# Performance work log

Hardware: AMD Instinct MI355X
Metric: run time of the kernel (lower is better)

## Reference

```python
import jax, jax.numpy as jnp
import numpy as np

N_QUBITS = 12
N_LAYERS = 6
BATCH = 512
DIM = 2 ** N_QUBITS


def _apply_1q(psi, G, wire):
    """Apply a single-qubit gate on `wire` (wire 0 = most significant).
    psi: [B, 2^n] complex. G: [2,2] (shared) or [B,2,2] (batched)."""
    B = psi.shape[0]
    left = 2 ** wire
    psi = psi.reshape(B, left, 2, -1)
    if G.ndim == 2:
        psi = jnp.einsum('ij,bxjy->bxiy', G, psi)
    else:
        psi = jnp.einsum('bij,bxjy->bxiy', G, psi)
    return psi.reshape(B, -1)


def _apply_cnot(psi, c, t):
    """CNOT with control c, target t on [B, 2^n] state."""
    B = psi.shape[0]
    ps = psi.reshape((B,) + (2,) * N_QUBITS)
    ca, ta = c + 1, t + 1
    c0 = jnp.take(ps, 0, axis=ca)
    c1 = jnp.take(ps, 1, axis=ca)
    flip_ax = ta if ta < ca else ta - 1
    c1 = jnp.flip(c1, axis=flip_ax)  # X on target within control=1 block
    ps = jnp.stack([c0, c1], axis=ca)
    return ps.reshape(B, -1)


def _circuit(x, weights):
    B = x.shape[0]
    psi = jnp.zeros((B, DIM), jnp.complex64).at[:, 0].set(1.0)

    # AngleEmbedding: RY(x_w) on each wire (batched gate matrices)
    h = 0.5 * x
    c, s = jnp.cos(h).astype(jnp.complex64), jnp.sin(h).astype(jnp.complex64)
    for w in range(N_QUBITS):
        G = jnp.stack([jnp.stack([c[:, w], -s[:, w]], -1),
                       jnp.stack([s[:, w], c[:, w]], -1)], -2)  # [B,2,2]
        psi = _apply_1q(psi, G, w)

    # StronglyEntanglingLayers: Rot(phi,theta,omega) per wire, then ring of CNOTs
    for l in range(N_LAYERS):
        phi, theta, omega = weights[l, :, 0], weights[l, :, 1], weights[l, :, 2]
        ct = jnp.cos(0.5 * theta).astype(jnp.complex64)
        st = jnp.sin(0.5 * theta).astype(jnp.complex64)
        ep = jnp.exp(-0.5j * (phi + omega).astype(jnp.complex64))
        em = jnp.exp(0.5j * (phi - omega).astype(jnp.complex64))
        # Rot = RZ(omega) RY(theta) RZ(phi)
        m00 = ep * ct
        m01 = -em * st
        m10 = jnp.conj(em) * st
        m11 = jnp.conj(ep) * ct
        for w in range(N_QUBITS):
            G = jnp.array([[m00[w], m01[w]], [m10[w], m11[w]]], jnp.complex64)
            psi = _apply_1q(psi, G, w)
        r = l % (N_QUBITS - 1) + 1
        for w in range(N_QUBITS):
            psi = _apply_cnot(psi, w, (w + r) % N_QUBITS)

    # <Z_w> for every wire
    probs = psi.real ** 2 + psi.imag ** 2  # [B, 2^n]
    exps = []
    for w in range(N_QUBITS):
        p = probs.reshape(B, 2 ** w, 2, -1)
        exps.append(p[:, :, 0, :].sum((1, 2)) - p[:, :, 1, :].sum((1, 2)))
    return jnp.stack(exps, -1)  # [B, n_qubits]


def setup_inputs() -> dict:
    key = jax.random.key(0)
    k1, k2, k3, k4 = jax.random.split(key, 4)
    x = jax.random.uniform(k1, (BATCH, N_QUBITS), jnp.float32, -np.pi, np.pi)
    weights = jax.random.uniform(k2, (N_LAYERS, N_QUBITS, 3), jnp.float32, 0.0, 2.0 * np.pi)
    W = jax.random.normal(k3, (1, N_QUBITS), jnp.float32) * 0.3
    b = jax.random.normal(k4, (1,), jnp.float32) * 0.01
    return {"x": x, "weights": weights, "W": W, "b": b}


def reference(x, weights, W, b):
    z = _circuit(x, weights)              # [B, n_qubits]
    y = z @ W.T + b                       # [B, 1]
    return y.squeeze(-1)                  # [B]
```

## Files before the change

kernel.cpp:

```cpp
#include <hip/hip_runtime.h>
#include <stdint.h>

#define NQ 12
#define DIM 4096
#define NLAYERS 6
#define TPB 512

typedef float v2f __attribute__((ext_vector_type(2)));

struct Pass_t {
    uint32_t WT[9];
    uint32_t WL[4];
    uint32_t RT[9];
    uint32_t RL[8];
};
struct Pass9_t {
    uint32_t WT[6];
    uint32_t WL[4];
    uint32_t RT[6];
    uint32_t RL[8];
};
struct CK_t {
    Pass9_t PA1;
    Pass9_t PA2;
    Pass_t PB;
    Pass_t P1[NLAYERS];
    uint32_t frow[NQ];
};

constexpr uint32_t S1f(uint32_t k){ return (k & 0xFC0u) | ((k & 7u) << 3) | ((k >> 3) & 7u); }
constexpr uint32_t S2f(uint32_t k){ return (k & 0xE38u) | ((k & 7u) << 6) | ((k >> 6) & 7u); }
constexpr uint32_t S3f(uint32_t k){ return (k & 0x1F8u) | ((k & 7u) << 9) | ((k >> 9) & 7u); }

constexpr uint32_t ech_reduce(const uint32_t* v, int n, uint32_t x){
    bool ch = true;
    while (ch) {
        ch = false;
        for (int i = 0; i < n; i++)
            if (v[i] && (x ^ v[i]) < x) { x ^= v[i]; ch = true; }
    }
    return x;
}

constexpr Pass_t build_pass(const uint32_t* Mc) {
    Pass_t P{};
    uint32_t rows[12]{};
    rows[0] = 4u;
    int nr = 1;
    uint32_t full[12]{}; int nf = 0; full[nf++] = 4u;
    uint32_t We[4]{};  int nw = 0;
    uint32_t Re[5]{};  int nre = 0;
    {
        uint32_t p0 = 0;
        for (int j = 0; j < 5; j++)
            p0 |= (uint32_t)(__builtin_popcount(4u & Mc[3 + j]) & 1) << j;
        uint32_t r = ech_reduce(Re, nre, p0);
        if (r) Re[nre++] = r;
    }
    for (int slot = 0; slot < 4; slot++) {
        uint32_t chosen = 0;
        for (int relax = 0; relax < 3 && !chosen; relax++) {
            for (uint32_t m = 1; m < 4096u && !chosen; m++) {
                if (m & 4u) continue;
                uint32_t wp = (m >> 3) & 15u;
                uint32_t wr = ech_reduce(We, nw, wp);
                if (relax < 2 && !wr) continue;
                uint32_t rp = 0;
                for (int j = 0; j < 5; j++)
                    rp |= (uint32_t)(__builtin_popcount(m & Mc[3 + j]) & 1) << j;
                uint32_t rr = ech_reduce(Re, nre, rp);
                if (relax < 1 && !rr) continue;
                uint32_t fr = ech_reduce(full, nf, m);
                if (!fr) continue;
                chosen = m; full[nf++] = fr;
                if (wr && nw < 4) We[nw++] = wr;
                if (rr && nre < 5) Re[nre++] = rr;
            }
        }
        rows[nr++] = chosen;
    }
    for (int slot = nr; slot < 12; slot++) {
        for (uint32_t m = 1; m < 4096u; m++) {
            if (m & 4u) continue;
            uint32_t fr = ech_reduce(full, nf, m);
            if (fr) { rows[slot] = m; full[nf++] = fr; break; }
        }
    }
    uint32_t col[12]{}, lmc[12]{};
    for (int j = 0; j < 12; j++) {
        uint32_t c = 0;
        for (int i = 0; i < 12; i++) c |= (uint32_t)((rows[i] >> j) & 1u) << i;
        col[j] = c;
    }
    for (int j = 0; j < 12; j++) {
        uint32_t a = 0, mc = Mc[j];
        for (int q = 0; q < 12; q++) if ((mc >> q) & 1u) a ^= col[q];
        lmc[j] = a;
    }
    for (int j = 0; j < 9; j++) { P.WT[j] = col[3 + j]; P.RT[j] = lmc[3 + j]; }
    for (int j = 0; j < 4; j++) {
        uint32_t a = 0;
        for (int q = 0; q < 2; q++) if ((j >> q) & 1) a ^= col[q];
        P.WL[j] = a;
    }
    for (int l = 0; l < 8; l++) {
        uint32_t a = 0;
        for (int q = 0; q < 3; q++) if ((l >> q) & 1) a ^= lmc[q];
        P.RL[l] = a;
    }
    return P;
}

constexpr Pass9_t build_pass9(const uint32_t* Mc) {
    Pass9_t P{};
    uint32_t rows[9]{};
    rows[0] = 4u;
    int nr = 1;
    uint32_t full[9]{}; int nf = 0; full[nf++] = 4u;
    uint32_t We[4]{};  int nw = 0;
    uint32_t Re[5]{};  int nre = 0;
    {
        uint32_t p0 = 0;
        for (int j = 0; j < 5; j++)
            p0 |= (uint32_t)(__builtin_popcount(4u & Mc[3 + j]) & 1) << j;
        uint32_t r = ech_reduce(Re, nre, p0);
        if (r) Re[nre++] = r;
    }
    for (int slot = 0; slot < 4; slot++) {
        uint32_t chosen = 0;
        for (int relax = 0; relax < 3 && !chosen; relax++) {
            for (uint32_t m = 1; m < 512u && !chosen; m++) {
                if (m & 4u) continue;
                uint32_t wp = (m >> 3) & 15u;
                uint32_t wr = ech_reduce(We, nw, wp);
                if (relax < 2 && !wr) continue;
                uint32_t rp = 0;
                for (int j = 0; j < 5; j++)
                    rp |= (uint32_t)(__builtin_popcount(m & Mc[3 + j]) & 1) << j;
                uint32_t rr = ech_reduce(Re, nre, rp);
                if (relax < 1 && !rr) continue;
                uint32_t fr = ech_reduce(full, nf, m);
                if (!fr) continue;
                chosen = m; full[nf++] = fr;
                if (wr && nw < 4) We[nw++] = wr;
                if (rr && nre < 5) Re[nre++] = rr;
            }
        }
        rows[nr++] = chosen;
    }
    for (int slot = nr; slot < 9; slot++) {
        for (uint32_t m = 1; m < 512u; m++) {
            if (m & 4u) continue;
            uint32_t fr = ech_reduce(full, nf, m);
            if (fr) { rows[slot] = m; full[nf++] = fr; break; }
        }
    }
    uint32_t col[9]{}, lmc[9]{};
    for (int j = 0; j < 9; j++) {
        uint32_t c = 0;
        for (int i = 0; i < 9; i++) c |= (uint32_t)((rows[i] >> j) & 1u) << i;
        col[j] = c;
    }
    for (int j = 0; j < 9; j++) {
        uint32_t a = 0, mc = Mc[j];
        for (int q = 0; q < 9; q++) if ((mc >> q) & 1u) a ^= col[q];
        lmc[j] = a;
    }
    for (int j = 0; j < 6; j++) { P.WT[j] = col[3 + j]; P.RT[j] = lmc[3 + j]; }
    for (int j = 0; j < 4; j++) {
        uint32_t a = 0;
        for (int q = 0; q < 2; q++) if ((j >> q) & 1) a ^= col[q];
        P.WL[j] = a;
    }
    for (int l = 0; l < 8; l++) {
        uint32_t a = 0;
        for (int q = 0; q < 3; q++) if ((l >> q) & 1) a ^= lmc[q];
        P.RL[l] = a;
    }
    return P;
}

constexpr CK_t build_ck() {
    CK_t ck{};
    uint32_t Acols[NLAYERS][NQ]{}, Aicol5[NQ]{};
    for (int l = 0; l < NLAYERS; l++) {
        int r = l % (NQ - 1) + 1;
        for (int q = 0; q < NQ; q++) {
            uint32_t v = 1u << q;
            for (int w = NQ - 1; w >= 0; w--) {
                int pc = NQ - 1 - w, pt = NQ - 1 - ((w + r) % NQ);
                v ^= ((v >> pc) & 1u) << pt;
            }
            Acols[l][q] = v;
            if (l == NLAYERS - 1) {
                uint32_t u = 1u << q;
                for (int w = 0; w < NQ; w++) {
                    int pc = NQ - 1 - w, pt = NQ - 1 - ((w + r) % NQ);
                    u ^= ((u >> pc) & 1u) << pt;
                }
                Aicol5[q] = u;
            }
        }
    }
    uint32_t Mc9[9]{};
    for (int j = 0; j < 9; j++) Mc9[j] = S1f(1u << j);
    ck.PA1 = build_pass9(Mc9);
    for (int j = 0; j < 9; j++) Mc9[j] = S2f(1u << j);
    ck.PA2 = build_pass9(Mc9);
    uint32_t Mc[12]{};
    for (int j = 0; j < 12; j++) Mc[j] = S3f(1u << j);
    ck.PB = build_pass(Mc);
    for (int l = 1; l < NLAYERS; l++) {
        for (int j = 0; j < 12; j++) Mc[j] = S3f(S2f(S1f(Acols[l - 1][j])));
        ck.P1[l] = build_pass(Mc);
    }
    uint32_t Mcol[NQ]{};
    for (int j = 0; j < NQ; j++) {
        uint32_t pj = S1f(S2f(S3f(1u << j)));
        uint32_t M = 0;
        for (int m = 0; m < NQ; m++) if ((pj >> m) & 1u) M ^= Aicol5[m];
        Mcol[j] = M;
    }
    for (int p = 0; p < NQ; p++) {
        uint32_t s = 0;
        for (int j = 0; j < NQ; j++) s |= ((Mcol[j] >> p) & 1u) << j;
        ck.frow[p] = s;
    }
    return ck;
}
constexpr CK_t CK = build_ck();

template<int Q>
__device__ __forceinline__ void gate_q(v2f (&PRE)[4], v2f (&PIM)[4], float4 m) {
    v2f bx = {m.x, m.x}, by = {m.y, m.y}, bz = {m.z, m.z}, bw = {m.w, m.w};
    #pragma unroll
    for (int j = 0; j < 4; j++) {
        if (j & (1 << Q)) continue;
        int j2 = j | (1 << Q);
        v2f re0 = PRE[j], im0 = PIM[j], re1 = PRE[j2], im1 = PIM[j2];
        PRE[j]  = __builtin_elementwise_fma(bx, re0,
                  __builtin_elementwise_fma(by, -im0,
                  __builtin_elementwise_fma(bz, re1, -bw * im1)));
        PIM[j]  = __builtin_elementwise_fma(bx, im0,
                  __builtin_elementwise_fma(by, re0,
                  __builtin_elementwise_fma(bz, im1, bw * re1)));
        PRE[j2] = __builtin_elementwise_fma(bx, re1,
                  __builtin_elementwise_fma(by, im1,
                  __builtin_elementwise_fma(bz, -re0, -bw * im0)));
        PIM[j2] = __builtin_elementwise_fma(bx, im1,
                  __builtin_elementwise_fma(by, -re1,
                  __builtin_elementwise_fma(bz, -im0, bw * re0)));
    }
}

__device__ __forceinline__ void pack_gate(v2f (&PRE)[4], v2f (&PIM)[4], float4 m) {
    v2f d1 = {-m.y, m.y}, d2 = {m.z, -m.z};
    #pragma unroll
    for (int j = 0; j < 4; j++) {
        v2f RE = PRE[j], IM = PIM[j];
        v2f sR = {RE.y, RE.x}, sI = {IM.y, IM.x};
        PRE[j] = m.x * RE + d1 * IM + d2 * sR - m.w * sI;
        PIM[j] = m.x * IM - d1 * RE + d2 * sI + m.w * sR;
    }
}

template<int IDX>
__device__ __forceinline__ void wl_pass(v2f (&PRE)[4], v2f (&PIM)[4],
                                        float* buf, uint32_t wb, uint32_t rb) {
    constexpr Pass9_t P = (IDX == 0) ? CK.PA1 : CK.PA2;
    v2f* bre = (v2f*)buf;
    v2f* bim = (v2f*)(buf + DIM);
    __asm__ volatile("s_waitcnt lgkmcnt(0)" ::: "memory");
    #pragma unroll
    for (int j = 0; j < 4; j++) {
        uint32_t s = (wb ^ P.WL[j]) >> 1;
        bre[s] = PRE[j]; bim[s] = PIM[j];
    }
    __asm__ volatile("s_waitcnt lgkmcnt(0)" ::: "memory");
    #pragma unroll
    for (int j = 0; j < 4; j++) {
        uint32_t s0 = rb ^ P.RL[j], s1 = rb ^ P.RL[j | 4];
        v2f re, im;
        re.x = buf[s0];       re.y = buf[s1];
        im.x = buf[DIM + s0]; im.y = buf[DIM + s1];
        PRE[j] = re; PIM[j] = im;
    }
}

__device__ __forceinline__ void p3_pass(v2f (&PRE)[4], v2f (&PIM)[4],
                                        float* buf, uint32_t wb, uint32_t rb) {
    constexpr Pass_t P = CK.PB;
    v2f* bre = (v2f*)buf;
    v2f* bim = (v2f*)(buf + DIM);
    __syncthreads();
    #pragma unroll
    for (int j = 0; j < 4; j++) {
        uint32_t s = (wb ^ P.WL[j]) >> 1;
        bre[s] = PRE[j]; bim[s] = PIM[j];
    }
    __syncthreads();
    #pragma unroll
    for (int j = 0; j < 4; j++) {
        uint32_t s0 = rb ^ P.RL[j], s1 = rb ^ P.RL[j | 4];
        v2f re, im;
        re.x = buf[s0];       re.y = buf[s1];
        im.x = buf[DIM + s0]; im.y = buf[DIM + s1];
        PRE[j] = re; PIM[j] = im;
    }
}

__device__ __forceinline__ void rebase_pass(v2f (&PRE)[4], v2f (&PIM)[4],
                                            float* buf, int tid, int l) {
    const Pass_t& P = CK.P1[l];
    uint32_t wb = 0, rb = 0;
    #pragma unroll
    for (int j = 0; j < 9; j++) {
        uint32_t sel = (uint32_t)(-(int)((tid >> j) & 1));
        wb ^= sel & P.WT[j];
        rb ^= sel & P.RT[j];
    }
    v2f* bre = (v2f*)buf;
    v2f* bim = (v2f*)(buf + DIM);
    #pragma unroll
    for (int j = 0; j < 4; j++) {
        uint32_t s = (wb ^ P.WL[j]) >> 1;
        bre[s] = PRE[j]; bim[s] = PIM[j];
    }
    __syncthreads();
    #pragma unroll
    for (int j = 0; j < 4; j++) {
        uint32_t s0 = rb ^ P.RL[j], s1 = rb ^ P.RL[j | 4];
        v2f re, im;
        re.x = buf[s0];       re.y = buf[s1];
        im.x = buf[DIM + s0]; im.y = buf[DIM + s1];
        PRE[j] = re; PIM[j] = im;
    }
}

__global__ __launch_bounds__(TPB, 4) void qsim_kernel(
    const float* __restrict__ x,
    const float* __restrict__ weights,
    const float* __restrict__ Wp,
    const float* __restrict__ bptr,
    float* __restrict__ out)
{
    __shared__ float  lds[2 * 2 * DIM];
    __shared__ float4 smat[NLAYERS * NQ];
    __shared__ float  scs[NQ], sss[NQ];
    __shared__ float  red[8];

    const int tid = threadIdx.x;
    const int b   = blockIdx.x;

    if (tid < NQ) {
        float s_, c_;
        sincosf(0.5f * x[b * NQ + tid], &s_, &c_);
        scs[tid] = c_; sss[tid] = s_;
    }
    if (tid < NLAYERS * NQ) {
        float phi   = weights[tid * 3 + 0];
        float theta = weights[tid * 3 + 1];
        float omega = weights[tid * 3 + 2];
        float st, ct; sincosf(0.5f * theta, &st, &ct);
        float sp, cp; sincosf(0.5f * (phi + omega), &sp, &cp);
        float sm, cm; sincosf(0.5f * (phi - omega), &sm, &cm);
        smat[tid] = make_float4(cp * ct, -sp * ct, -cm * st, -sm * st);
    }
    __syncthreads();

    float base = 1.0f;
    #pragma unroll
    for (int t = 0; t < 9; t++) {
        int w = 8 - t;
        base *= ((tid >> t) & 1) ? sss[w] : scs[w];
    }
    v2f PRE[4], PIM[4];
    float c9 = scs[9], s9 = sss[9];
    #pragma unroll
    for (int j = 0; j < 4; j++) {
        float a = base;
        #pragma unroll
        for (int p = 0; p < 2; p++) {
            int w = NQ - 1 - p;
            a *= ((j >> p) & 1) ? sss[w] : scs[w];
        }
        PRE[j].x = a * c9;  PRE[j].y = a * s9;
        PIM[j].x = 0.0f;    PIM[j].y = 0.0f;
    }

    uint32_t p1wb = 0, p1rb = 0, p2wb = 0, p2rb = 0, p3wb = 0, p3rb = 0;
    #pragma unroll
    for (int j = 0; j < 6; j++) {
        uint32_t sel = (uint32_t)(-(int)((tid >> j) & 1));
        p1wb ^= sel & CK.PA1.WT[j]; p1rb ^= sel & CK.PA1.RT[j];
        p2wb ^= sel & CK.PA2.WT[j]; p2rb ^= sel & CK.PA2.RT[j];
    }
    #pragma unroll
    for (int j = 0; j < 9; j++) {
        uint32_t sel = (uint32_t)(-(int)((tid >> j) & 1));
        p3wb ^= sel & CK.PB.WT[j]; p3rb ^= sel & CK.PB.RT[j];
    }
    {
        uint32_t wvb = (uint32_t)(tid & 0x1C0) << 3;
        p1wb |= wvb; p1rb |= wvb; p2wb |= wvb; p2rb |= wvb;
    }

    float* bufA = lds;
    float* bufB = lds + 2 * DIM;

    #pragma clang loop unroll(disable)
    for (int l = 0; l < NLAYERS; l++) {
        if (l > 0) rebase_pass(PRE, PIM, bufB, tid, l);
        const int sb = l * NQ;
        gate_q<0>(PRE, PIM, smat[sb + 11]);
        gate_q<1>(PRE, PIM, smat[sb + 10]);
        pack_gate(PRE, PIM, smat[sb + 9]);
        wl_pass<0>(PRE, PIM, bufA, p1wb, p1rb);
        gate_q<0>(PRE, PIM, smat[sb + 8]);
        gate_q<1>(PRE, PIM, smat[sb + 7]);
        pack_gate(PRE, PIM, smat[sb + 6]);
        wl_pass<1>(PRE, PIM, bufA, p2wb, p2rb);
        gate_q<0>(PRE, PIM, smat[sb + 5]);
        gate_q<1>(PRE, PIM, smat[sb + 4]);
        pack_gate(PRE, PIM, smat[sb + 3]);
        p3_pass(PRE, PIM, bufA, p3wb, p3rb);
        gate_q<0>(PRE, PIM, smat[sb + 2]);
        gate_q<1>(PRE, PIM, smat[sb + 1]);
        pack_gate(PRE, PIM, smat[sb + 0]);
    }

    const float bv = bptr[0];
    float wbT[NQ];
    #pragma unroll
    for (int p = 0; p < NQ; p++) {
        uint32_t row = CK.frow[p];
        int tp = __popc(tid & (int)(row >> 3)) & 1;
        float Wv = Wp[NQ - 1 - p];
        wbT[p] = tp ? -Wv : Wv;
    }
    v2f acc2 = {0.0f, 0.0f};
    #pragma unroll
    for (int j = 0; j < 4; j++) {
        float cx = bv, cy = bv;
        #pragma unroll
        for (int p = 0; p < NQ; p++) {
            uint32_t row = CK.frow[p];
            float s = (__popc(j & (int)(row & 3u)) & 1) ? -wbT[p] : wbT[p];
            cx += s;
            cy += (row & 4u) ? -s : s;
        }
        v2f c = {cx, cy};
        acc2 += (PRE[j] * PRE[j] + PIM[j] * PIM[j]) * c;
    }
    float acc = acc2.x + acc2.y;
    #pragma unroll
    for (int off = 32; off > 0; off >>= 1)
        acc += __shfl_down(acc, off, 64);
    if ((tid & 63) == 0) red[tid >> 6] = acc;
    __syncthreads();
    if (tid == 0) {
        float r = 0.0f;
        #pragma unroll
        for (int wv = 0; wv < 8; wv++) r += red[wv];
        out[b] = r;
    }
}

extern "C" void kernel_launch(void* const* d_in, const int* in_sizes, int n_in,
                              void* d_out, int out_size, void* d_ws, size_t ws_size,
                              hipStream_t stream) {
    const float* x       = (const float*)d_in[0];
    const float* weights = (const float*)d_in[1];
    const float* W       = (const float*)d_in[2];
    const float* bptr    = (const float*)d_in[3];
    qsim_kernel<<<512, TPB, 0, stream>>>(x, weights, W, bptr, (float*)d_out);
}
```

Baseline: 90.72 us.

## Replace intra-wave LDS transposes with DPP, swizzle and permlane swaps

Replaces the two warp-local LDS write/read passes in each layer with register-level exchanges using DPP quad permutes, ds_swizzle and permlane16/32 swaps. The qubit-to-lane mapping (S1f) and the gate order for wires 6 and 7 are changed to match the new lane permutation. The leading __syncthreads in p3_pass is also dropped. The aim is to cut LDS traffic and waitcnt stalls, at the cost of many cross-lane instructions and a risk to correctness if the bit mapping or barrier removal is wrong.

```diff
diff --git a/kernel.cpp b/kernel.cpp
--- a/kernel.cpp
+++ b/kernel.cpp
@@ -14,21 +14,21 @@
     uint32_t RT[9];
     uint32_t RL[8];
 };
-struct Pass9_t {
-    uint32_t WT[6];
-    uint32_t WL[4];
-    uint32_t RT[6];
-    uint32_t RL[8];
-};
 struct CK_t {
-    Pass9_t PA1;
-    Pass9_t PA2;
     Pass_t PB;
     Pass_t P1[NLAYERS];
     uint32_t frow[NQ];
 };
 
-constexpr uint32_t S1f(uint32_t k){ return (k & 0xFC0u) | ((k & 7u) << 3) | ((k >> 3) & 7u); }
+constexpr uint32_t S1f(uint32_t k){
+    return (k & 0xFC0u)
+         |  ((k >> 3) & 1u)
+         | (((k >> 5) & 1u) << 1)
+         | (((k >> 4) & 1u) << 2)
+         | (( k       & 1u) << 3)
+         | (((k >> 2) & 1u) << 4)
+         | (((k >> 1) & 1u) << 5);
+}
 constexpr uint32_t S2f(uint32_t k){ return (k & 0xE38u) | ((k & 7u) << 6) | ((k >> 6) & 7u); }
 constexpr uint32_t S3f(uint32_t k){ return (k & 0x1F8u) | ((k & 7u) << 9) | ((k >> 9) & 7u); }
 
@@ -111,75 +111,6 @@
     return P;
 }
 
-constexpr Pass9_t build_pass9(const uint32_t* Mc) {
-    Pass9_t P{};
-    uint32_t rows[9]{};
-    rows[0] = 4u;
-    int nr = 1;
-    uint32_t full[9]{}; int nf = 0; full[nf++] = 4u;
-    uint32_t We[4]{};  int nw = 0;
-    uint32_t Re[5]{};  int nre = 0;
-    {
-        uint32_t p0 = 0;
-        for (int j = 0; j < 5; j++)
-            p0 |= (uint32_t)(__builtin_popcount(4u & Mc[3 + j]) & 1) << j;
-        uint32_t r = ech_reduce(Re, nre, p0);
-        if (r) Re[nre++] = r;
-    }
-    for (int slot = 0; slot < 4; slot++) {
-        uint32_t chosen = 0;
-        for (int relax = 0; relax < 3 && !chosen; relax++) {
-            for (uint32_t m = 1; m < 512u && !chosen; m++) {
-                if (m & 4u) continue;
-                uint32_t wp = (m >> 3) & 15u;
-                uint32_t wr = ech_reduce(We, nw, wp);
-                if (relax < 2 && !wr) continue;
-                uint32_t rp = 0;
-                for (int j = 0; j < 5; j++)
-                    rp |= (uint32_t)(__builtin_popcount(m & Mc[3 + j]) & 1) << j;
-                uint32_t rr = ech_reduce(Re, nre, rp);
-                if (relax < 1 && !rr) continue;
-                uint32_t fr = ech_reduce(full, nf, m);
-                if (!fr) continue;
-                chosen = m; full[nf++] = fr;
-                if (wr && nw < 4) We[nw++] = wr;
-                if (rr && nre < 5) Re[nre++] = rr;
-            }
-        }
-        rows[nr++] = chosen;
-    }
-    for (int slot = nr; slot < 9; slot++) {
-        for (uint32_t m = 1; m < 512u; m++) {
-            if (m & 4u) continue;
-            uint32_t fr = ech_reduce(full, nf, m);
-            if (fr) { rows[slot] = m; full[nf++] = fr; break; }
-        }
-    }
-    uint32_t col[9]{}, lmc[9]{};
-    for (int j = 0; j < 9; j++) {
-        uint32_t c = 0;
-        for (int i = 0; i < 9; i++) c |= (uint32_t)((rows[i] >> j) & 1u) << i;
-        col[j] = c;
-    }
-    for (int j = 0; j < 9; j++) {
-        uint32_t a = 0, mc = Mc[j];
-        for (int q = 0; q < 9; q++) if ((mc >> q) & 1u) a ^= col[q];
-        lmc[j] = a;
-    }
-    for (int j = 0; j < 6; j++) { P.WT[j] = col[3 + j]; P.RT[j] = lmc[3 + j]; }
-    for (int j = 0; j < 4; j++) {
-        uint32_t a = 0;
-        for (int q = 0; q < 2; q++) if ((j >> q) & 1) a ^= col[q];
-        P.WL[j] = a;
-    }
-    for (int l = 0; l < 8; l++) {
-        uint32_t a = 0;
-        for (int q = 0; q < 3; q++) if ((l >> q) & 1) a ^= lmc[q];
-        P.RL[l] = a;
-    }
-    return P;
-}
-
 constexpr CK_t build_ck() {
     CK_t ck{};
     uint32_t Acols[NLAYERS][NQ]{}, Aicol5[NQ]{};
@@ -202,11 +133,6 @@
             }
         }
     }
-    uint32_t Mc9[9]{};
-    for (int j = 0; j < 9; j++) Mc9[j] = S1f(1u << j);
-    ck.PA1 = build_pass9(Mc9);
-    for (int j = 0; j < 9; j++) Mc9[j] = S2f(1u << j);
-    ck.PA2 = build_pass9(Mc9);
     uint32_t Mc[12]{};
     for (int j = 0; j < 12; j++) Mc[j] = S3f(1u << j);
     ck.PB = build_pass(Mc);
@@ -264,27 +190,73 @@
     }
 }
 
-template<int IDX>
-__device__ __forceinline__ void wl_pass(v2f (&PRE)[4], v2f (&PIM)[4],
-                                        float* buf, uint32_t wb, uint32_t rb) {
-    constexpr Pass9_t P = (IDX == 0) ? CK.PA1 : CK.PA2;
-    v2f* bre = (v2f*)buf;
-    v2f* bim = (v2f*)(buf + DIM);
-    __asm__ volatile("s_waitcnt lgkmcnt(0)" ::: "memory");
-    #pragma unroll
-    for (int j = 0; j < 4; j++) {
-        uint32_t s = (wb ^ P.WL[j]) >> 1;
-        bre[s] = PRE[j]; bim[s] = PIM[j];
-    }
-    __asm__ volatile("s_waitcnt lgkmcnt(0)" ::: "memory");
-    #pragma unroll
-    for (int j = 0; j < 4; j++) {
-        uint32_t s0 = rb ^ P.RL[j], s1 = rb ^ P.RL[j | 4];
-        v2f re, im;
-        re.x = buf[s0];       re.y = buf[s1];
-        im.x = buf[DIM + s0]; im.y = buf[DIM + s1];
-        PRE[j] = re; PIM[j] = im;
-    }
+template<int CTRL>
+__device__ __forceinline__ float dpp_f(float v) {
+    return __int_as_float(__builtin_amdgcn_mov_dpp(__float_as_int(v), CTRL, 0xF, 0xF, false));
+}
+template<int OFF>
+__device__ __forceinline__ float swz_f(float v) {
+    return __int_as_float(__builtin_amdgcn_ds_swizzle(__float_as_int(v), OFF));
+}
+
+#define QSWAP(CTRL, A, B, HI) do {                                   \
+    float _ta = dpp_f<CTRL>(A), _tb = dpp_f<CTRL>(B);                \
+    float _na = (HI) ? _tb : (A);                                    \
+    float _nb = (HI) ? (B) : _ta;                                    \
+    (A) = _na; (B) = _nb;                                            \
+} while (0)
+
+#define SSWAP(OFF, A, B, HI) do {                                    \
+    float _s = (HI) ? (A) : (B);                                     \
+    float _t = swz_f<OFF>(_s);                                       \
+    float _na = (HI) ? _t : (A);                                     \
+    float _nb = (HI) ? (B) : _t;                                     \
+    (A) = _na; (B) = _nb;                                            \
+} while (0)
+
+#define PLSWAP32(A, B) do {                                          \
+    auto _r = __builtin_amdgcn_permlane32_swap(                      \
+        __float_as_int(A), __float_as_int(B), false, false);         \
+    (A) = __int_as_float(_r[0]); (B) = __int_as_float(_r[1]);        \
+} while (0)
+#define PLSWAP16(A, B) do {                                          \
+    auto _r = __builtin_amdgcn_permlane16_swap(                      \
+        __float_as_int(A), __float_as_int(B), false, false);         \
+    (A) = __int_as_float(_r[0]); (B) = __int_as_float(_r[1]);        \
+} while (0)
+
+__device__ __forceinline__ void trans1(v2f (&PRE)[4], v2f (&PIM)[4], int tid) {
+    const bool h0 = (tid & 1);
+    const bool h1 = (tid & 2);
+    const bool h2 = (tid & 4);
+    QSWAP(0xB1, PRE[0].x, PRE[1].x, h0); QSWAP(0xB1, PRE[2].x, PRE[3].x, h0);
+    QSWAP(0xB1, PRE[0].y, PRE[1].y, h0); QSWAP(0xB1, PRE[2].y, PRE[3].y, h0);
+    QSWAP(0xB1, PIM[0].x, PIM[1].x, h0); QSWAP(0xB1, PIM[2].x, PIM[3].x, h0);
+    QSWAP(0xB1, PIM[0].y, PIM[1].y, h0); QSWAP(0xB1, PIM[2].y, PIM[3].y, h0);
+    SSWAP(0x101F, PRE[0].x, PRE[2].x, h2); SSWAP(0x101F, PRE[1].x, PRE[3].x, h2);
+    SSWAP(0x101F, PRE[0].y, PRE[2].y, h2); SSWAP(0x101F, PRE[1].y, PRE[3].y, h2);
+    SSWAP(0x101F, PIM[0].x, PIM[2].x, h2); SSWAP(0x101F, PIM[1].x, PIM[3].x, h2);
+    SSWAP(0x101F, PIM[0].y, PIM[2].y, h2); SSWAP(0x101F, PIM[1].y, PIM[3].y, h2);
+    QSWAP(0x4E, PRE[0].x, PRE[0].y, h1); QSWAP(0x4E, PRE[1].x, PRE[1].y, h1);
+    QSWAP(0x4E, PRE[2].x, PRE[2].y, h1); QSWAP(0x4E, PRE[3].x, PRE[3].y, h1);
+    QSWAP(0x4E, PIM[0].x, PIM[0].y, h1); QSWAP(0x4E, PIM[1].x, PIM[1].y, h1);
+    QSWAP(0x4E, PIM[2].x, PIM[2].y, h1); QSWAP(0x4E, PIM[3].x, PIM[3].y, h1);
+}
+
+__device__ __forceinline__ void trans2(v2f (&PRE)[4], v2f (&PIM)[4], int tid) {
+    const bool h3 = (tid & 8);
+    SSWAP(0x201F, PRE[0].x, PRE[1].x, h3); SSWAP(0x201F, PRE[2].x, PRE[3].x, h3);
+    SSWAP(0x201F, PRE[0].y, PRE[1].y, h3); SSWAP(0x201F, PRE[2].y, PRE[3].y, h3);
+    SSWAP(0x201F, PIM[0].x, PIM[1].x, h3); SSWAP(0x201F, PIM[2].x, PIM[3].x, h3);
+    SSWAP(0x201F, PIM[0].y, PIM[1].y, h3); SSWAP(0x201F, PIM[2].y, PIM[3].y, h3);
+    PLSWAP16(PRE[0].x, PRE[2].x); PLSWAP16(PRE[1].x, PRE[3].x);
+    PLSWAP16(PRE[0].y, PRE[2].y); PLSWAP16(PRE[1].y, PRE[3].y);
+    PLSWAP16(PIM[0].x, PIM[2].x); PLSWAP16(PIM[1].x, PIM[3].x);
+    PLSWAP16(PIM[0].y, PIM[2].y); PLSWAP16(PIM[1].y, PIM[3].y);
+    PLSWAP32(PRE[0].x, PRE[0].y); PLSWAP32(PRE[1].x, PRE[1].y);
+    PLSWAP32(PRE[2].x, PRE[2].y); PLSWAP32(PRE[3].x, PRE[3].y);
+    PLSWAP32(PIM[0].x, PIM[0].y); PLSWAP32(PIM[1].x, PIM[1].y);
+    PLSWAP32(PIM[2].x, PIM[2].y); PLSWAP32(PIM[3].x, PIM[3].y);
 }
 
 __device__ __forceinline__ void p3_pass(v2f (&PRE)[4], v2f (&PIM)[4],
@@ -292,7 +264,6 @@
     constexpr Pass_t P = CK.PB;
     v2f* bre = (v2f*)buf;
     v2f* bim = (v2f*)(buf + DIM);
-    __syncthreads();
     #pragma unroll
     for (int j = 0; j < 4; j++) {
         uint32_t s = (wb ^ P.WL[j]) >> 1;
@@ -388,21 +359,11 @@
         PIM[j].x = 0.0f;    PIM[j].y = 0.0f;
     }
 
-    uint32_t p1wb = 0, p1rb = 0, p2wb = 0, p2rb = 0, p3wb = 0, p3rb = 0;
-    #pragma unroll
-    for (int j = 0; j < 6; j++) {
-        uint32_t sel = (uint32_t)(-(int)((tid >> j) & 1));
-        p1wb ^= sel & CK.PA1.WT[j]; p1rb ^= sel & CK.PA1.RT[j];
-        p2wb ^= sel & CK.PA2.WT[j]; p2rb ^= sel & CK.PA2.RT[j];
-    }
+    uint32_t p3wb = 0, p3rb = 0;
     #pragma unroll
     for (int j = 0; j < 9; j++) {
         uint32_t sel = (uint32_t)(-(int)((tid >> j) & 1));
         p3wb ^= sel & CK.PB.WT[j]; p3rb ^= sel & CK.PB.RT[j];
-    }
-    {
-        uint32_t wvb = (uint32_t)(tid & 0x1C0) << 3;
-        p1wb |= wvb; p1rb |= wvb; p2wb |= wvb; p2rb |= wvb;
     }
 
     float* bufA = lds;
@@ -415,11 +376,11 @@
         gate_q<0>(PRE, PIM, smat[sb + 11]);
         gate_q<1>(PRE, PIM, smat[sb + 10]);
         pack_gate(PRE, PIM, smat[sb + 9]);
-        wl_pass<0>(PRE, PIM, bufA, p1wb, p1rb);
+        trans1(PRE, PIM, tid);
         gate_q<0>(PRE, PIM, smat[sb + 8]);
-        gate_q<1>(PRE, PIM, smat[sb + 7]);
-        pack_gate(PRE, PIM, smat[sb + 6]);
-        wl_pass<1>(PRE, PIM, bufA, p2wb, p2rb);
+        gate_q<1>(PRE, PIM, smat[sb + 6]);
+        pack_gate(PRE, PIM, smat[sb + 7]);
+        trans2(PRE, PIM, tid);
         gate_q<0>(PRE, PIM, smat[sb + 5]);
         gate_q<1>(PRE, PIM, smat[sb + 4]);
         pack_gate(PRE, PIM, smat[sb + 3]);
```

Result: slower. 92.86 us (+2.4%).

## Process two batch states per block and interleave their gate and exchange phases

Applied to the files above, without the earlier changes.

Each block now simulates two batch elements, launching 256 blocks instead of 512. The gate windows of state B are interleaved with the block-wide LDS exchanges of state A, and vice versa, so that one state's barrier latency can be hidden by the other's arithmetic. It uses separate cross-wave LDS buffers per state plus a shared wave-local buffer, which raises LDS per block to 48KB. It also doubles register state and lowers the launch-bounds occupancy hint from 4 to 2, so occupancy and parallelism across the GPU drop.

```diff
diff --git a/kernel.cpp b/kernel.cpp
--- a/kernel.cpp
+++ b/kernel.cpp
@@ -264,6 +264,12 @@
     }
 }
 
+__device__ __forceinline__ void win(v2f (&PRE)[4], v2f (&PIM)[4], const float4* p) {
+    gate_q<0>(PRE, PIM, p[2]);
+    gate_q<1>(PRE, PIM, p[1]);
+    pack_gate(PRE, PIM, p[0]);
+}
+
 template<int IDX>
 __device__ __forceinline__ void wl_pass(v2f (&PRE)[4], v2f (&PIM)[4],
                                         float* buf, uint32_t wb, uint32_t rb) {
@@ -287,21 +293,21 @@
     }
 }
 
-__device__ __forceinline__ void p3_pass(v2f (&PRE)[4], v2f (&PIM)[4],
-                                        float* buf, uint32_t wb, uint32_t rb) {
-    constexpr Pass_t P = CK.PB;
+__device__ __forceinline__ void cross_w(const v2f (&PRE)[4], const v2f (&PIM)[4],
+                                        float* buf, uint32_t wb, const uint32_t* WL) {
     v2f* bre = (v2f*)buf;
     v2f* bim = (v2f*)(buf + DIM);
-    __syncthreads();
-    #pragma unroll
-    for (int j = 0; j < 4; j++) {
-        uint32_t s = (wb ^ P.WL[j]) >> 1;
+    #pragma unroll
+    for (int j = 0; j < 4; j++) {
+        uint32_t s = (wb ^ WL[j]) >> 1;
         bre[s] = PRE[j]; bim[s] = PIM[j];
     }
-    __syncthreads();
-    #pragma unroll
-    for (int j = 0; j < 4; j++) {
-        uint32_t s0 = rb ^ P.RL[j], s1 = rb ^ P.RL[j | 4];
+}
+__device__ __forceinline__ void cross_r(v2f (&PRE)[4], v2f (&PIM)[4],
+                                        const float* buf, uint32_t rb, const uint32_t* RL) {
+    #pragma unroll
+    for (int j = 0; j < 4; j++) {
+        uint32_t s0 = rb ^ RL[j], s1 = rb ^ RL[j | 4];
         v2f re, im;
         re.x = buf[s0];       re.y = buf[s1];
         im.x = buf[DIM + s0]; im.y = buf[DIM + s1];
@@ -309,53 +315,54 @@
     }
 }
 
-__device__ __forceinline__ void rebase_pass(v2f (&PRE)[4], v2f (&PIM)[4],
-                                            float* buf, int tid, int l) {
-    const Pass_t& P = CK.P1[l];
-    uint32_t wb = 0, rb = 0;
-    #pragma unroll
-    for (int j = 0; j < 9; j++) {
-        uint32_t sel = (uint32_t)(-(int)((tid >> j) & 1));
-        wb ^= sel & P.WT[j];
-        rb ^= sel & P.RT[j];
-    }
-    v2f* bre = (v2f*)buf;
-    v2f* bim = (v2f*)(buf + DIM);
-    #pragma unroll
-    for (int j = 0; j < 4; j++) {
-        uint32_t s = (wb ^ P.WL[j]) >> 1;
-        bre[s] = PRE[j]; bim[s] = PIM[j];
-    }
-    __syncthreads();
-    #pragma unroll
-    for (int j = 0; j < 4; j++) {
-        uint32_t s0 = rb ^ P.RL[j], s1 = rb ^ P.RL[j | 4];
-        v2f re, im;
-        re.x = buf[s0];       re.y = buf[s1];
-        im.x = buf[DIM + s0]; im.y = buf[DIM + s1];
-        PRE[j] = re; PIM[j] = im;
-    }
-}
-
-__global__ __launch_bounds__(TPB, 4) void qsim_kernel(
+__device__ __forceinline__ void init_state(v2f (&PRE)[4], v2f (&PIM)[4],
+                                           const float* scs, const float* sss, int tid) {
+    float base = 1.0f;
+    #pragma unroll
+    for (int t = 0; t < 9; t++) {
+        int w = 8 - t;
+        base *= ((tid >> t) & 1) ? sss[w] : scs[w];
+    }
+    float c9 = scs[9], s9 = sss[9];
+    #pragma unroll
+    for (int j = 0; j < 4; j++) {
+        float a = base;
+        #pragma unroll
+        for (int p = 0; p < 2; p++) {
+            int w = NQ - 1 - p;
+            a *= ((j >> p) & 1) ? sss[w] : scs[w];
+        }
+        PRE[j].x = a * c9;  PRE[j].y = a * s9;
+        PIM[j].x = 0.0f;    PIM[j].y = 0.0f;
+    }
+}
+
+__global__ __launch_bounds__(TPB, 2) void qsim_kernel(
     const float* __restrict__ x,
     const float* __restrict__ weights,
     const float* __restrict__ Wp,
     const float* __restrict__ bptr,
     float* __restrict__ out)
 {
-    __shared__ float  lds[2 * 2 * DIM];
+    __shared__ float  lds[3 * 2 * DIM];
     __shared__ float4 smat[NLAYERS * NQ];
-    __shared__ float  scs[NQ], sss[NQ];
-    __shared__ float  red[8];
+    __shared__ float  scsA[NQ], sssA[NQ], scsB[NQ], sssB[NQ];
+    __shared__ float  red[16];
 
     const int tid = threadIdx.x;
     const int b   = blockIdx.x;
+    const int bA  = 2 * b, bB = 2 * b + 1;
 
     if (tid < NQ) {
         float s_, c_;
-        sincosf(0.5f * x[b * NQ + tid], &s_, &c_);
-        scs[tid] = c_; sss[tid] = s_;
+        sincosf(0.5f * x[bA * NQ + tid], &s_, &c_);
+        scsA[tid] = c_; sssA[tid] = s_;
+    }
+    if (tid >= 64 && tid < 64 + NQ) {
+        int q = tid - 64;
+        float s_, c_;
+        sincosf(0.5f * x[bB * NQ + q], &s_, &c_);
+        scsB[q] = c_; sssB[q] = s_;
     }
     if (tid < NLAYERS * NQ) {
         float phi   = weights[tid * 3 + 0];
@@ -368,25 +375,9 @@
     }
     __syncthreads();
 
-    float base = 1.0f;
-    #pragma unroll
-    for (int t = 0; t < 9; t++) {
-        int w = 8 - t;
-        base *= ((tid >> t) & 1) ? sss[w] : scs[w];
-    }
-    v2f PRE[4], PIM[4];
-    float c9 = scs[9], s9 = sss[9];
-    #pragma unroll
-    for (int j = 0; j < 4; j++) {
-        float a = base;
-        #pragma unroll
-        for (int p = 0; p < 2; p++) {
-            int w = NQ - 1 - p;
-            a *= ((j >> p) & 1) ? sss[w] : scs[w];
-        }
-        PRE[j].x = a * c9;  PRE[j].y = a * s9;
-        PIM[j].x = 0.0f;    PIM[j].y = 0.0f;
-    }
+    v2f PRA[4], PIA[4], PRB[4], PIB[4];
+    init_state(PRA, PIA, scsA, sssA, tid);
+    init_state(PRB, PIB, scsB, sssB, tid);
 
     uint32_t p1wb = 0, p1rb = 0, p2wb = 0, p2rb = 0, p3wb = 0, p3rb = 0;
     #pragma unroll
@@ -405,29 +396,62 @@
         p1wb |= wvb; p1rb |= wvb; p2wb |= wvb; p2rb |= wvb;
     }
 
-    float* bufA = lds;
-    float* bufB = lds + 2 * DIM;
+    float* wl   = lds;
+    float* bufXA = lds + 2 * DIM;
+    float* bufXB = lds + 4 * DIM;
+
+    win(PRA, PIA, &smat[9]);  wl_pass<0>(PRA, PIA, wl, p1wb, p1rb);
+    win(PRA, PIA, &smat[6]);  wl_pass<1>(PRA, PIA, wl, p2wb, p2rb);
+    win(PRB, PIB, &smat[9]);  wl_pass<0>(PRB, PIB, wl, p1wb, p1rb);
+    win(PRA, PIA, &smat[3]);
+    cross_w(PRA, PIA, bufXA, p3wb, CK.PB.WL);
+    __syncthreads();
+    cross_r(PRA, PIA, bufXA, p3rb, CK.PB.RL);
+    win(PRB, PIB, &smat[6]);  wl_pass<1>(PRB, PIB, wl, p2wb, p2rb);
+    win(PRA, PIA, &smat[0]);
+    win(PRB, PIB, &smat[3]);
+    cross_w(PRB, PIB, bufXB, p3wb, CK.PB.WL);
+    __syncthreads();
+    cross_r(PRB, PIB, bufXB, p3rb, CK.PB.RL);
 
     #pragma clang loop unroll(disable)
-    for (int l = 0; l < NLAYERS; l++) {
-        if (l > 0) rebase_pass(PRE, PIM, bufB, tid, l);
-        const int sb = l * NQ;
-        gate_q<0>(PRE, PIM, smat[sb + 11]);
-        gate_q<1>(PRE, PIM, smat[sb + 10]);
-        pack_gate(PRE, PIM, smat[sb + 9]);
-        wl_pass<0>(PRE, PIM, bufA, p1wb, p1rb);
-        gate_q<0>(PRE, PIM, smat[sb + 8]);
-        gate_q<1>(PRE, PIM, smat[sb + 7]);
-        pack_gate(PRE, PIM, smat[sb + 6]);
-        wl_pass<1>(PRE, PIM, bufA, p2wb, p2rb);
-        gate_q<0>(PRE, PIM, smat[sb + 5]);
-        gate_q<1>(PRE, PIM, smat[sb + 4]);
-        pack_gate(PRE, PIM, smat[sb + 3]);
-        p3_pass(PRE, PIM, bufA, p3wb, p3rb);
-        gate_q<0>(PRE, PIM, smat[sb + 2]);
-        gate_q<1>(PRE, PIM, smat[sb + 1]);
-        pack_gate(PRE, PIM, smat[sb + 0]);
-    }
+    for (int l = 1; l < NLAYERS; l++) {
+        const Pass_t& P = CK.P1[l];
+        uint32_t rwb = 0, rrb = 0;
+        #pragma unroll
+        for (int j = 0; j < 9; j++) {
+            uint32_t sel = (uint32_t)(-(int)((tid >> j) & 1));
+            rwb ^= sel & P.WT[j];
+            rrb ^= sel & P.RT[j];
+        }
+        const int sb = l * NQ, sp = (l - 1) * NQ;
+
+        cross_w(PRA, PIA, bufXA, rwb, P.WL);
+        __syncthreads();
+        cross_r(PRA, PIA, bufXA, rrb, P.RL);
+        win(PRB, PIB, &smat[sp + 0]);
+        win(PRA, PIA, &smat[sb + 9]);
+        wl_pass<0>(PRA, PIA, wl, p1wb, p1rb);
+        cross_w(PRB, PIB, bufXB, rwb, P.WL);
+        __syncthreads();
+        cross_r(PRB, PIB, bufXB, rrb, P.RL);
+        win(PRA, PIA, &smat[sb + 6]);
+        wl_pass<1>(PRA, PIA, wl, p2wb, p2rb);
+        win(PRB, PIB, &smat[sb + 9]);
+        wl_pass<0>(PRB, PIB, wl, p1wb, p1rb);
+        win(PRA, PIA, &smat[sb + 3]);
+        cross_w(PRA, PIA, bufXA, p3wb, CK.PB.WL);
+        __syncthreads();
+        cross_r(PRA, PIA, bufXA, p3rb, CK.PB.RL);
+        win(PRB, PIB, &smat[sb + 6]);
+        wl_pass<1>(PRB, PIB, wl, p2wb, p2rb);
+        win(PRA, PIA, &smat[sb + 0]);
+        win(PRB, PIB, &smat[sb + 3]);
+        cross_w(PRB, PIB, bufXB, p3wb, CK.PB.WL);
+        __syncthreads();
+        cross_r(PRB, PIB, bufXB, p3rb, CK.PB.RL);
+    }
+    win(PRB, PIB, &smat[5 * NQ + 0]);
 
     const float bv = bptr[0];
     float wbT[NQ];
@@ -438,7 +462,7 @@
         float Wv = Wp[NQ - 1 - p];
         wbT[p] = tp ? -Wv : Wv;
     }
-    v2f acc2 = {0.0f, 0.0f};
+    v2f accA2 = {0.0f, 0.0f}, accB2 = {0.0f, 0.0f};
     #pragma unroll
     for (int j = 0; j < 4; j++) {
         float cx = bv, cy = bv;
@@ -450,19 +474,32 @@
             cy += (row & 4u) ? -s : s;
         }
         v2f c = {cx, cy};
-        acc2 += (PRE[j] * PRE[j] + PIM[j] * PIM[j]) * c;
-    }
-    float acc = acc2.x + acc2.y;
-    #pragma unroll
-    for (int off = 32; off > 0; off >>= 1)
-        acc += __shfl_down(acc, off, 64);
-    if ((tid & 63) == 0) red[tid >> 6] = acc;
+        accA2 += (PRA[j] * PRA[j] + PIA[j] * PIA[j]) * c;
+        accB2 += (PRB[j] * PRB[j] + PIB[j] * PIB[j]) * c;
+    }
+    float accA = accA2.x + accA2.y;
+    float accB = accB2.x + accB2.y;
+    #pragma unroll
+    for (int off = 32; off > 0; off >>= 1) {
+        accA += __shfl_down(accA, off, 64);
+        accB += __shfl_down(accB, off, 64);
+    }
+    if ((tid & 63) == 0) {
+        red[tid >> 6]     = accA;
+        red[(tid >> 6) + 8] = accB;
+    }
     __syncthreads();
     if (tid == 0) {
         float r = 0.0f;
         #pragma unroll
         for (int wv = 0; wv < 8; wv++) r += red[wv];
-        out[b] = r;
+        out[bA] = r;
+    }
+    if (tid == 1) {
+        float r = 0.0f;
+        #pragma unroll
+        for (int wv = 0; wv < 8; wv++) r += red[wv + 8];
+        out[bB] = r;
     }
 }
 
@@ -473,5 +510,5 @@
     const float* weights = (const float*)d_in[1];
     const float* W       = (const float*)d_in[2];
     const float* bptr    = (const float*)d_in[3];
-    qsim_kernel<<<512, TPB, 0, stream>>>(x, weights, W, bptr, (float*)d_out);
-}
+    qsim_kernel<<<256, TPB, 0, stream>>>(x, weights, W, bptr, (float*)d_out);
+}
```

After: 92.93 us. 2.4% more time.
